# Optimization experiments

Hardware: AMD Instinct MI355X
Metric: run time of the kernel (lower is better)

## Reference

```python
import jax, jax.numpy as jnp
import numpy as np


def setup_inputs() -> dict:
    key = jax.random.key(0)
    ks = jax.random.split(key, 6)
    B, T, C = 1, 2048, 2048
    Hq, Hkv = 32, 8
    D = C // Hq  # 64
    s = 0.02  # weight init scale for numerical stability
    return {
        "x": jax.random.normal(ks[0], (B, T, C), dtype=jnp.float32),
        "Wq": jax.random.normal(ks[1], (C, C), dtype=jnp.float32) * s,
        "Wk": jax.random.normal(ks[2], (Hkv * D, C), dtype=jnp.float32) * s,
        "Wv": jax.random.normal(ks[3], (Hkv * D, C), dtype=jnp.float32) * s,
        "Wo": jax.random.normal(ks[4], (C, C), dtype=jnp.float32) * s,
        "bo": jnp.zeros((C,), dtype=jnp.float32),
        "num_query_heads": Hq,
        "num_kv_heads": Hkv,
    }


def reference(x, Wq, Wk, Wv, Wo, bo, num_query_heads, num_kv_heads):
    B, T, C = x.shape
    Hq, Hkv = num_query_heads, num_kv_heads
    D = C // Hq
    G = Hq // Hkv  # queries per kv head

    q = (x @ Wq.T).reshape(B, T, Hkv, G, D)   # grouped query heads
    k = (x @ Wk.T).reshape(B, T, Hkv, D)
    v = (x @ Wv.T).reshape(B, T, Hkv, D)

    scale = 1.0 / jnp.sqrt(jnp.asarray(D, dtype=x.dtype))
    # [B, Hkv, G, T, T]; KV head broadcast over group dim instead of repeat_interleave
    scores = jnp.einsum("bthgd,bshd->bhgts", q, k) * scale

    causal = jnp.tril(jnp.ones((T, T), dtype=bool))  # allow j <= i
    scores = jnp.where(causal, scores, jnp.asarray(-jnp.inf, dtype=scores.dtype))
    attn = jax.nn.softmax(scores, axis=-1)  # dropout is identity at p=0.0 / eval

    out = jnp.einsum("bhgts,bshd->bthgd", attn, v).reshape(B, T, C)
    return out @ Wo.T + bo
```

## Files before the change

kernel.cpp:

```cpp
#include <hip/hip_runtime.h>
#include <hip/hip_bf16.h>

typedef __attribute__((ext_vector_type(8))) short short8;
typedef __attribute__((ext_vector_type(16))) float floatx16;
typedef __attribute__((ext_vector_type(4))) float floatx4;
typedef __attribute__((ext_vector_type(4))) unsigned uintx4;

template<int N> struct IC { static constexpr int v = N; };

__device__ __forceinline__ short f2bf(float f) {
    unsigned u = __builtin_bit_cast(unsigned, f);
    u += 0x7fffu + ((u >> 16) & 1u);
    return (short)(u >> 16);
}

__device__ __forceinline__ unsigned pk_bf16(float lo, float hi) {
    unsigned short a = __builtin_bit_cast(unsigned short, (__bf16)lo);
    unsigned short b = __builtin_bit_cast(unsigned short, (__bf16)hi);
    return (unsigned)a | ((unsigned)b << 16);
}

__device__ __forceinline__ void gload_lds16(const void* g, void* l) {
    __builtin_amdgcn_global_load_lds(
        (const __attribute__((address_space(1))) unsigned*)g,
        (__attribute__((address_space(3))) unsigned*)l, 16, 0, 0);
}

__global__ __launch_bounds__(256)
void convsw(const float* __restrict__ src, short* __restrict__ dst) {
    const int row = blockIdx.x;
    const int c = threadIdx.x;
    const int kt = c >> 3, cc = c & 7;
    const float* s = src + (size_t)row * 2048 + kt * 64 + (cc ^ (row & 7)) * 8;
    float4 v0 = *(const float4*)s;
    float4 v1 = *(const float4*)(s + 4);
    short8 o = { f2bf(v0.x), f2bf(v0.y), f2bf(v0.z), f2bf(v0.w),
                 f2bf(v1.x), f2bf(v1.y), f2bf(v1.z), f2bf(v1.w) };
    *(short8*)(dst + (size_t)row * 2048 + kt * 64 + cc * 8) = o;
}

__global__ __launch_bounds__(256)
void conv_all(const float* __restrict__ x, const float* __restrict__ Wq,
              const float* __restrict__ Wk, const float* __restrict__ Wv,
              short* __restrict__ xb, short* __restrict__ wqkv) {
    const int bid = blockIdx.x;
    const float* src; short* dst; int srow, drow;
    if (bid < 2048)      { src = x;  dst = xb;   srow = bid;        drow = bid; }
    else {
        int r = bid - 2048;
        dst = wqkv; drow = r;
        if (r < 2048)      { src = Wq; srow = r; }
        else if (r < 2560) { src = Wk; srow = r - 2048; }
        else               { src = Wv; srow = r - 2560; }
    }
    const int c = threadIdx.x;
    const int kt = c >> 3, cc = c & 7;
    const float* s = src + (size_t)srow * 2048 + kt * 64 + (cc ^ (drow & 7)) * 8;
    float4 v0 = *(const float4*)s;
    float4 v1 = *(const float4*)(s + 4);
    short8 o = { f2bf(v0.x), f2bf(v0.y), f2bf(v0.z), f2bf(v0.w),
                 f2bf(v1.x), f2bf(v1.y), f2bf(v1.z), f2bf(v1.w) };
    *(short8*)(dst + (size_t)drow * 2048 + kt * 64 + cc * 8) = o;
}

template<int BN, int EPI>
__global__ __launch_bounds__(512, 4)
void gemm8(const short* __restrict__ A, const short* __restrict__ Bw,
           short* __restrict__ qb, short* __restrict__ kb, short* __restrict__ vt,
           float* __restrict__ fout, const float* __restrict__ bias) {
    constexpr int K = 2048;
    constexpr int NN = BN / 32;
    constexpr int ACH = 128 * 8;
    constexpr int NCH = (128 + BN) * 8;
    __shared__ short sm[2][(128 + BN) * 64];

    const int t = threadIdx.x, lane = t & 63, w = t >> 6;
    const int wm = w & 3, wn = w >> 2;
    const int l15 = lane & 15, lh = lane >> 4;
    const int bn = blockIdx.x, bm = blockIdx.y;
    const int ra0 = bm * 128;
    const short* Bbase = Bw + (size_t)bn * BN * K;

    floatx4 acc[2][NN] = {};

    auto stage = [&](int buf, int k0) {
        short* base = &sm[buf][0];
        #pragma unroll
        for (int i = 0; i < NCH / 512; ++i) {
            int c = i * 512 + t;
            if (c < ACH) {
                int row = c >> 3, cc = c & 7;
                gload_lds16(A + (size_t)(ra0 + row) * K + k0 + cc * 8, base + c * 8);
            } else {
                int c2 = c - ACH;
                int row = c2 >> 3, cc = c2 & 7;
                gload_lds16(Bbase + (size_t)row * K + k0 + cc * 8, base + (ACH + c2) * 8);
            }
        }
    };

    stage(0, 0);
    #pragma unroll 1
    for (int it = 0; it < K / 64; ++it) {
        __syncthreads();
        if (it + 1 < K / 64) stage((it + 1) & 1, (it + 1) * 64);
        const short* As = &sm[it & 1][0];
        const short* Bs = As + 128 * 64;
        #pragma unroll
        for (int kf = 0; kf < 2; ++kf) {
            short8 a[2], b[NN];
            #pragma unroll
            for (int m = 0; m < 2; ++m) {
                int arow = wm * 32 + m * 16 + l15;
                a[m] = *(const short8*)(As + arow * 64 + (((kf * 4 + lh) ^ (arow & 7)) << 3));
            }
            #pragma unroll
            for (int n = 0; n < NN; ++n) {
                int brow = wn * (BN / 2) + n * 16 + l15;
                b[n] = *(const short8*)(Bs + brow * 64 + (((kf * 4 + lh) ^ (brow & 7)) << 3));
            }
            #pragma unroll
            for (int m = 0; m < 2; ++m)
                #pragma unroll
                for (int n = 0; n < NN; ++n)
                    acc[m][n] = __builtin_amdgcn_mfma_f32_16x16x32_bf16(a[m], b[n], acc[m][n], 0, 0, 0);
        }
    }

    #pragma unroll
    for (int m = 0; m < 2; ++m) {
        #pragma unroll
        for (int n = 0; n < NN; ++n) {
            #pragma unroll
            for (int r = 0; r < 4; ++r) {
                int row = ra0 + wm * 32 + m * 16 + lh * 4 + r;
                int col = bn * BN + wn * (BN / 2) + n * 16 + l15;
                float v = acc[m][n][r];
                if constexpr (EPI == 1) {
                    fout[(size_t)row * 2048 + col] = v + bias[col];
                } else {
                    if (col < 2048) {
                        qb[(size_t)row * 2048 + col] = f2bf(v * 0.18033688011112042f);
                    } else if (col < 2560) {
                        int kcol = col - 2048, within = kcol & 63;
                        int cp = ((within >> 3) ^ (row & 7)) & 7;
                        kb[(size_t)row * 512 + (kcol & ~63) + (cp << 3) + (within & 7)] = f2bf(v);
                    } else {
                        int dg = col - 2560;
                        int cp = (((row >> 3) & 7) ^ (dg & 7)) & 7;
                        vt[(size_t)dg * 2048 + (row & ~63) + (cp << 3) + (row & 7)] = f2bf(v);
                    }
                }
            }
        }
    }
}

__global__ __launch_bounds__(512, 4)
void attn_fwd(const short* __restrict__ qb, const short* __restrict__ kb,
              const short* __restrict__ vt, short* __restrict__ ob) {
    __shared__ __align__(16) short smem[2][16384];

    const int t = threadIdx.x, lane = t & 63, w = t >> 6;
    const int l31 = lane & 31, hi = lane >> 5;
    const int pairi = blockIdx.x;
    const int hq = blockIdx.y, hk = hq >> 2;
    const int qtA = pairi, qtB = 31 - pairi;
    const int a = w >> 1, p = w & 1;
    const int s = a & 1, h = a >> 1;
    const int tile1 = (a < 2) ? qtA : qtB;
    const int swl = l31 & 7;

    int rg = tile1 * 64 + s * 32 + l31;

    short8 qf[4];
    {
        const short* qrow = qb + (size_t)rg * 2048 + hq * 64;
        #pragma unroll
        for (int kk = 0; kk < 4; ++kk)
            qf[kk] = *(const short8*)(qrow + kk * 16 + hi * 8);
    }

    float m = -3e38f, l = 0.f;
    floatx16 acc[2] = {};

    auto stage = [&](int buf, int j0) {
        short* base = &smem[buf][0];
        #pragma unroll
        for (int i = 0; i < 4; ++i) {
            int c = i * 512 + t;
            if (i < 2) {
                int row = c >> 3, cc = c & 7;
                gload_lds16(kb + (size_t)(j0 + row) * 512 + hk * 64 + cc * 8, base + c * 8);
            } else {
                int cv = c - 1024, drow = cv >> 4, cc = cv & 15;
                gload_lds16(vt + (size_t)(hk * 64 + drow) * 2048 + j0 + cc * 8, base + c * 8);
            }
        }
    };

    auto save_part = [&](float* mb) {
        #pragma unroll
        for (int n = 0; n < 2; ++n)
            #pragma unroll
            for (int r = 0; r < 16; ++r) mb[n * 16 + r] = acc[n][r];
        mb[32] = m;
        mb[33] = l;
    };
    auto merge_part = [&](const float* mb) {
        float m1 = mb[32], l1 = mb[33];
        float M = fmaxf(m, m1);
        float sf0 = __builtin_amdgcn_exp2f(m - M);
        float sf1 = __builtin_amdgcn_exp2f(m1 - M);
        l = sf0 * l + sf1 * l1;
        #pragma unroll
        for (int n = 0; n < 2; ++n)
            #pragma unroll
            for (int r = 0; r < 16; ++r)
                acc[n][r] = sf0 * acc[n][r] + sf1 * mb[n * 16 + r];
        m = M;
    };
    auto writeout = [&](int rgw) {
        const float linv = 1.0f / l;
        const int sw8 = rgw & 7;
        #pragma unroll
        for (int n = 0; n < 2; ++n) {
            #pragma unroll
            for (int g = 0; g < 4; ++g) {
                #pragma unroll
                for (int e = 0; e < 4; e += 2) {
                    int r = 4 * g + e;
                    unsigned pkv = pk_bf16(acc[n][r] * linv, acc[n][r + 1] * linv);
                    int d = 32 * n + e + 8 * g + 4 * hi;
                    int col = hq * 64 + d;
                    int cp = ((col >> 3) & 7) ^ sw8;
                    *(unsigned*)(ob + (size_t)rgw * 2048 + (col & ~63) + (cp << 3) + (col & 7)) = pkv;
                }
            }
        }
    };

    auto process = [&](const short* K0, const short* V0, int blk0, auto NB,
                       int kt, bool diag) {
        constexpr int nblk = decltype(NB)::v;
        floatx16 sT[nblk];
        #pragma unroll
        for (int ib = 0; ib < nblk; ++ib) {
            floatx16 a2 = {};
            const int row = p * 64 + (blk0 + ib) * 32 + l31;
            #pragma unroll
            for (int kk = 0; kk < 4; ++kk) {
                short8 kf = *(const short8*)(K0 + row * 64 + (((2 * kk + hi) ^ swl) << 3));
                a2 = __builtin_amdgcn_mfma_f32_32x32x16_bf16(kf, qf[kk], a2, 0, 0, 0);
            }
            sT[ib] = a2;
        }
        if (diag) {
            #pragma unroll
            for (int ib = 0; ib < nblk; ++ib)
                #pragma unroll
                for (int r = 0; r < 16; ++r) {
                    int jg = kt * 64 + (blk0 + ib) * 32 + (r & 3) + 8 * (r >> 2) + 4 * hi;
                    if (jg > rg) sT[ib][r] = -3e38f;
                }
        }
        float v[16];
        #pragma unroll
        for (int r = 0; r < 16; ++r) {
            v[r] = sT[0][r];
            if constexpr (nblk == 2) v[r] = fmaxf(v[r], sT[1][r]);
        }
        #pragma unroll
        for (int st = 8; st >= 1; st >>= 1)
            #pragma unroll
            for (int r = 0; r < 8; ++r)
                if (r < st) v[r] = fmaxf(v[r], v[r + st]);
        float tm = fmaxf(v[0], __shfl_xor(v[0], 32));

        if (!__all(tm <= m + 8.0f)) {
            float mn = fmaxf(m, tm);
            float sf = __builtin_amdgcn_exp2f(m - mn);
            m = mn;
            l *= sf;
            #pragma unroll
            for (int n = 0; n < 2; ++n)
                #pragma unroll
                for (int r = 0; r < 16; ++r) acc[n][r] *= sf;
        }

        float sv[16];
        #pragma unroll
        for (int ib = 0; ib < nblk; ++ib)
            #pragma unroll
            for (int r = 0; r < 16; ++r)
                sT[ib][r] = __builtin_amdgcn_exp2f(sT[ib][r] - m);
        #pragma unroll
        for (int r = 0; r < 16; ++r) {
            sv[r] = sT[0][r];
            if constexpr (nblk == 2) sv[r] += sT[1][r];
        }
        #pragma unroll
        for (int st = 8; st >= 1; st >>= 1)
            #pragma unroll
            for (int r = 0; r < 8; ++r)
                if (r < st) sv[r] += sv[r + st];
        l += sv[0] + __shfl_xor(sv[0], 32);

        #pragma unroll
        for (int ib = 0; ib < nblk; ++ib) {
            unsigned Qd[8], Pd[8];
            #pragma unroll
            for (int c = 0; c < 8; ++c)
                Qd[c] = pk_bf16(sT[ib][2 * c], sT[ib][2 * c + 1]);
            #pragma unroll
            for (int c = 0; c < 8; ++c)
                Pd[c] = __shfl_xor(Qd[c], 32);
            #pragma unroll
            for (int b = 0; b < 2; ++b) {
                uintx4 j;
                if (b == 0) {
                    j.x = hi ? Pd[2] : Qd[0];
                    j.y = hi ? Pd[3] : Qd[1];
                    j.z = hi ? Qd[2] : Pd[0];
                    j.w = hi ? Qd[3] : Pd[1];
                } else {
                    j.x = hi ? Pd[6] : Qd[4];
                    j.y = hi ? Pd[7] : Qd[5];
                    j.z = hi ? Qd[6] : Pd[4];
                    j.w = hi ? Qd[7] : Pd[5];
                }
                short8 pf = __builtin_bit_cast(short8, j);
                const int kk = (blk0 + ib) * 2 + b;
                const int ch = p * 64 + (((2 * kk + hi) ^ swl) << 3);
                short8 vf0 = *(const short8*)(V0 + l31 * 128 + ch);
                acc[0] = __builtin_amdgcn_mfma_f32_32x32x16_bf16(vf0, pf, acc[0], 0, 0, 0);
                short8 vf1 = *(const short8*)(V0 + (32 + l31) * 128 + ch);
                acc[1] = __builtin_amdgcn_mfma_f32_32x32x16_bf16(vf1, pf, acc[1], 0, 0, 0);
            }
        }
    };

    const int ss_tr = (qtA >> 1) + 1;
    const int nss = (qtB >> 1) + 1;

    stage(0, 0);
    for (int ss = 0; ss < ss_tr; ++ss) {
        __syncthreads();
        if (ss + 1 < ss_tr) stage((ss + 1) & 1, (ss + 1) * 128);
        const int kt = 2 * ss + p;
        if (kt <= tile1)
            process(&smem[ss & 1][0], &smem[ss & 1][8192], 0, IC<2>{}, kt, kt == tile1);
    }

    __syncthreads();
    stage(ss_tr & 1, ss_tr * 128);
    {
        float* msc = (float*)&smem[(ss_tr - 1) & 1][0];
        if (a < 2 && p == 1) save_part(msc + (s * 64 + lane) * 34);
        __syncthreads();
        if (a < 2 && p == 0) {
            merge_part(msc + (s * 64 + lane) * 34);
            writeout(rg);
        }
        if (a < 2) {
            rg = qtB * 64 + s * 32 + l31;
            const short* qrow = qb + (size_t)rg * 2048 + hq * 64;
            #pragma unroll
            for (int kk = 0; kk < 4; ++kk)
                qf[kk] = *(const short8*)(qrow + kk * 16 + hi * 8);
            m = -3e38f;
            l = 0.f;
            acc[0] = (floatx16){};
            acc[1] = (floatx16){};
        }
    }

    for (int ss = ss_tr; ss < nss; ++ss) {
        __syncthreads();
        if (ss + 1 < nss) stage((ss + 1) & 1, (ss + 1) * 128);
        const int kt = 2 * ss + p;
        if (kt <= qtB)
            process(&smem[ss & 1][0], &smem[ss & 1][8192], h, IC<1>{}, kt, kt == qtB);
    }

    __syncthreads();
    float* msc = (float*)&smem[0][0];
    if (p == 1) save_part(msc + (a * 64 + lane) * 34);
    __syncthreads();
    if (p == 0) merge_part(msc + (a * 64 + lane) * 34);
    __syncthreads();
    if (p == 0 && a >= 2) save_part(msc + ((a & 1) * 64 + lane) * 34);
    __syncthreads();
    if (p == 0 && a < 2) {
        merge_part(msc + (a * 64 + lane) * 34);
        writeout(rg);
    }
}

extern "C" void kernel_launch(void* const* d_in, const int* in_sizes, int n_in,
                              void* d_out, int out_size, void* d_ws, size_t ws_size,
                              hipStream_t stream) {
    const float* x  = (const float*)d_in[0];
    const float* Wq = (const float*)d_in[1];
    const float* Wk = (const float*)d_in[2];
    const float* Wv = (const float*)d_in[3];
    const float* Wo = (const float*)d_in[4];
    const float* bo = (const float*)d_in[5];

    char* ws = (char*)d_ws;
    short* xb   = (short*)ws;
    short* wqkv = (short*)(ws + ((size_t)8  << 20));
    short* qb   = (short*)(ws + ((size_t)20 << 20));
    short* kb   = (short*)(ws + ((size_t)28 << 20));
    short* vt   = (short*)(ws + ((size_t)30 << 20));
    short* ob   = xb;
    short* wob  = wqkv;

    conv_all<<<5120, 256, 0, stream>>>(x, Wq, Wk, Wv, xb, wqkv);
    gemm8<128, 0><<<dim3(24, 16), 512, 0, stream>>>(xb, wqkv, qb, kb, vt, nullptr, nullptr);
    convsw<<<2048, 256, 0, stream>>>(Wo, wob);
    attn_fwd<<<dim3(16, 32), 512, 0, stream>>>(qb, kb, vt, ob);
    gemm8<64, 1><<<dim3(32, 16), 512, 0, stream>>>(ob, wob, nullptr, nullptr, nullptr,
                                                   (float*)d_out, bo);
}
```

Measured before the change: 122.0 us.

## Deepen LDS prefetch with vmcnt barriers, merge Wo conversion, add setprio

The GEMM and attention kernels now prefetch two stages ahead and wait with partial vmcnt counts plus raw barriers instead of a full __syncthreads. This keeps global-to-LDS loads in flight while MFMAs run. The Wo conversion kernel is folded into conv_all, writing to its own workspace region, which drops one launch. Attention also reverses tile pairing for half the heads and raises wave priority around MFMA sections. Hand-tuned vmcnt thresholds and the staging skip conditions are fragile and could cause races if the count of loads per stage changes.

```diff
diff --git a/kernel.cpp b/kernel.cpp
--- a/kernel.cpp
+++ b/kernel.cpp
@@ -26,33 +26,42 @@
         (__attribute__((address_space(3))) unsigned*)l, 16, 0, 0);
 }
 
-__global__ __launch_bounds__(256)
-void convsw(const float* __restrict__ src, short* __restrict__ dst) {
-    const int row = blockIdx.x;
-    const int c = threadIdx.x;
-    const int kt = c >> 3, cc = c & 7;
-    const float* s = src + (size_t)row * 2048 + kt * 64 + (cc ^ (row & 7)) * 8;
-    float4 v0 = *(const float4*)s;
-    float4 v1 = *(const float4*)(s + 4);
-    short8 o = { f2bf(v0.x), f2bf(v0.y), f2bf(v0.z), f2bf(v0.w),
-                 f2bf(v1.x), f2bf(v1.y), f2bf(v1.z), f2bf(v1.w) };
-    *(short8*)(dst + (size_t)row * 2048 + kt * 64 + cc * 8) = o;
+__device__ __forceinline__ void bar_vm4() {
+    asm volatile("s_waitcnt vmcnt(4)" ::: "memory");
+    __builtin_amdgcn_s_barrier();
+    __builtin_amdgcn_sched_barrier(0);
+}
+__device__ __forceinline__ void bar_vm3() {
+    asm volatile("s_waitcnt vmcnt(3)" ::: "memory");
+    __builtin_amdgcn_s_barrier();
+    __builtin_amdgcn_sched_barrier(0);
+}
+__device__ __forceinline__ void bar_vm0() {
+    asm volatile("s_waitcnt vmcnt(0)" ::: "memory");
+    __builtin_amdgcn_s_barrier();
+    __builtin_amdgcn_sched_barrier(0);
+}
+__device__ __forceinline__ void bar_raw() {
+    __builtin_amdgcn_sched_barrier(0);
+    __builtin_amdgcn_s_barrier();
+    __builtin_amdgcn_sched_barrier(0);
 }
 
 __global__ __launch_bounds__(256)
 void conv_all(const float* __restrict__ x, const float* __restrict__ Wq,
               const float* __restrict__ Wk, const float* __restrict__ Wv,
-              short* __restrict__ xb, short* __restrict__ wqkv) {
+              const float* __restrict__ Wo, short* __restrict__ xb,
+              short* __restrict__ wqkv, short* __restrict__ wob) {
     const int bid = blockIdx.x;
     const float* src; short* dst; int srow, drow;
-    if (bid < 2048)      { src = x;  dst = xb;   srow = bid;        drow = bid; }
-    else {
+    if (bid < 2048)      { src = x;  dst = xb;  srow = bid;        drow = bid; }
+    else if (bid < 5120) {
         int r = bid - 2048;
         dst = wqkv; drow = r;
         if (r < 2048)      { src = Wq; srow = r; }
         else if (r < 2560) { src = Wk; srow = r - 2048; }
         else               { src = Wv; srow = r - 2560; }
-    }
+    } else               { src = Wo; dst = wob; srow = bid - 5120; drow = srow; }
     const int c = threadIdx.x;
     const int kt = c >> 3, cc = c & 7;
     const float* s = src + (size_t)srow * 2048 + kt * 64 + (cc ^ (drow & 7)) * 8;
@@ -72,6 +81,7 @@
     constexpr int NN = BN / 32;
     constexpr int ACH = 128 * 8;
     constexpr int NCH = (128 + BN) * 8;
+    constexpr int NIT = K / 64;
     __shared__ short sm[2][(128 + BN) * 64];
 
     const int t = threadIdx.x, lane = t & 63, w = t >> 6;
@@ -100,10 +110,12 @@
     };
 
     stage(0, 0);
+    stage(1, 64);
     #pragma unroll 1
-    for (int it = 0; it < K / 64; ++it) {
-        __syncthreads();
-        if (it + 1 < K / 64) stage((it + 1) & 1, (it + 1) * 64);
+    for (int it = 0; it < NIT; ++it) {
+        if (it < NIT - 1) {
+            if constexpr (BN == 128) bar_vm4(); else bar_vm3();
+        } else bar_vm0();
         const short* As = &sm[it & 1][0];
         const short* Bs = As + 128 * 64;
         #pragma unroll
@@ -125,6 +137,8 @@
                 for (int n = 0; n < NN; ++n)
                     acc[m][n] = __builtin_amdgcn_mfma_f32_16x16x32_bf16(a[m], b[n], acc[m][n], 0, 0, 0);
         }
+        bar_raw();
+        if (it + 2 < NIT) stage(it & 1, (it + 2) * 64);
     }
 
     #pragma unroll
@@ -163,8 +177,8 @@
 
     const int t = threadIdx.x, lane = t & 63, w = t >> 6;
     const int l31 = lane & 31, hi = lane >> 5;
-    const int pairi = blockIdx.x;
     const int hq = blockIdx.y, hk = hq >> 2;
+    const int pairi = (hq < 16) ? blockIdx.x : 15 - blockIdx.x;
     const int qtA = pairi, qtB = 31 - pairi;
     const int a = w >> 1, p = w & 1;
     const int s = a & 1, h = a >> 1;
@@ -244,6 +258,7 @@
                        int kt, bool diag) {
         constexpr int nblk = decltype(NB)::v;
         floatx16 sT[nblk];
+        __builtin_amdgcn_s_setprio(1);
         #pragma unroll
         for (int ib = 0; ib < nblk; ++ib) {
             floatx16 a2 = {};
@@ -255,6 +270,7 @@
             }
             sT[ib] = a2;
         }
+        __builtin_amdgcn_s_setprio(0);
         if (diag) {
             #pragma unroll
             for (int ib = 0; ib < nblk; ++ib)
@@ -315,6 +331,7 @@
             #pragma unroll
             for (int c = 0; c < 8; ++c)
                 Pd[c] = __shfl_xor(Qd[c], 32);
+            __builtin_amdgcn_s_setprio(1);
             #pragma unroll
             for (int b = 0; b < 2; ++b) {
                 uintx4 j;
@@ -337,6 +354,7 @@
                 short8 vf1 = *(const short8*)(V0 + (32 + l31) * 128 + ch);
                 acc[1] = __builtin_amdgcn_mfma_f32_32x32x16_bf16(vf1, pf, acc[1], 0, 0, 0);
             }
+            __builtin_amdgcn_s_setprio(0);
         }
     };
 
@@ -344,18 +362,21 @@
     const int nss = (qtB >> 1) + 1;
 
     stage(0, 0);
+    stage(1, 128);
+
+    #pragma unroll 1
     for (int ss = 0; ss < ss_tr; ++ss) {
-        __syncthreads();
-        if (ss + 1 < ss_tr) stage((ss + 1) & 1, (ss + 1) * 128);
+        if (ss < nss - 1) bar_vm4(); else bar_vm0();
         const int kt = 2 * ss + p;
         if (kt <= tile1)
             process(&smem[ss & 1][0], &smem[ss & 1][8192], 0, IC<2>{}, kt, kt == tile1);
+        bar_raw();
+        if (ss + 2 < nss && ss + 2 != ss_tr + 1) stage(ss & 1, (ss + 2) * 128);
     }
 
     __syncthreads();
-    stage(ss_tr & 1, ss_tr * 128);
     {
-        float* msc = (float*)&smem[(ss_tr - 1) & 1][0];
+        float* msc = (float*)&smem[(ss_tr + 1) & 1][0];
         if (a < 2 && p == 1) save_part(msc + (s * 64 + lane) * 34);
         __syncthreads();
         if (a < 2 && p == 0) {
@@ -373,14 +394,18 @@
             acc[0] = (floatx16){};
             acc[1] = (floatx16){};
         }
-    }
-
+        __syncthreads();
+        if (ss_tr + 1 < nss) stage((ss_tr + 1) & 1, (ss_tr + 1) * 128);
+    }
+
+    #pragma unroll 1
     for (int ss = ss_tr; ss < nss; ++ss) {
-        __syncthreads();
-        if (ss + 1 < nss) stage((ss + 1) & 1, (ss + 1) * 128);
+        if (ss < nss - 1) bar_vm4(); else bar_vm0();
         const int kt = 2 * ss + p;
         if (kt <= qtB)
             process(&smem[ss & 1][0], &smem[ss & 1][8192], h, IC<1>{}, kt, kt == qtB);
+        bar_raw();
+        if (ss + 2 < nss) stage(ss & 1, (ss + 2) * 128);
     }
 
     __syncthreads();
@@ -413,12 +438,11 @@
     short* qb   = (short*)(ws + ((size_t)20 << 20));
     short* kb   = (short*)(ws + ((size_t)28 << 20));
     short* vt   = (short*)(ws + ((size_t)30 << 20));
+    short* wob  = (short*)(ws + ((size_t)32 << 20));
     short* ob   = xb;
-    short* wob  = wqkv;
-
-    conv_all<<<5120, 256, 0, stream>>>(x, Wq, Wk, Wv, xb, wqkv);
+
+    conv_all<<<7168, 256, 0, stream>>>(x, Wq, Wk, Wv, Wo, xb, wqkv, wob);
     gemm8<128, 0><<<dim3(24, 16), 512, 0, stream>>>(xb, wqkv, qb, kb, vt, nullptr, nullptr);
-    convsw<<<2048, 256, 0, stream>>>(Wo, wob);
     attn_fwd<<<dim3(16, 32), 512, 0, stream>>>(qb, kb, vt, ob);
     gemm8<64, 1><<<dim3(32, 16), 512, 0, stream>>>(ob, wob, nullptr, nullptr, nullptr,
                                                    (float*)d_out, bo);
```

Result: slower. 125.0 us (+2.4%).
